# Kernel optimization log

Hardware: AMD Instinct MI355X
Metric: run time of the kernel (lower is better)

Reference implementation:

```python
import jax, jax.numpy as jnp
import numpy as np

H, C = 4, 32  # heads, per-head out_channels; hidden = H*C = 128


def _gatv2(x, Wl, bl, Wr, br, att, b, src, dst):
    """One PyG GATv2Conv layer (concat=True, add_self_loops=False, slope=0.2)."""
    N = x.shape[0]
    xl = (x @ Wl + bl).reshape(N, H, C)  # source transform (messages)
    xr = (x @ Wr + br).reshape(N, H, C)  # target transform
    msg = xl[src]                         # [E,H,C] gather per edge
    e = jax.nn.leaky_relu(msg + xr[dst], 0.2)
    a = jnp.einsum('ehc,hc->eh', e, att)  # [E,H] attention logits
    # segment softmax over incoming edges of each target node
    amax = jax.ops.segment_max(a, dst, num_segments=N)
    a = jnp.exp(a - amax[dst])
    denom = jax.ops.segment_sum(a, dst, num_segments=N)
    a = a / (denom[dst] + 1e-16)
    out = jax.ops.segment_sum(a[..., None] * msg, dst, num_segments=N)  # [N,H,C]
    return out.reshape(N, H * C) + b


def setup_inputs() -> dict:
    key = jax.random.key(0)
    ks = jax.random.split(key, 16)
    N, E, F = 50000, 800000, H * C
    s = 1.0 / np.sqrt(F)
    inp = {
        'x': jax.random.normal(ks[0], (N, F), dtype=jnp.float32),
        'edge_index': jax.random.randint(ks[1], (2, E), 0, N, dtype=jnp.int32),
    }
    names = ['Wl1', 'Wr1', 'Wl2', 'Wr2']
    for i, n in enumerate(names):
        inp[n] = jax.random.normal(ks[2 + i], (F, F), dtype=jnp.float32) * s
    inp['bl1'] = jnp.zeros((F,), jnp.float32)
    inp['br1'] = jnp.zeros((F,), jnp.float32)
    inp['bl2'] = jnp.zeros((F,), jnp.float32)
    inp['br2'] = jnp.zeros((F,), jnp.float32)
    inp['att1'] = jax.random.normal(ks[6], (H, C), dtype=jnp.float32) * s
    inp['att2'] = jax.random.normal(ks[7], (H, C), dtype=jnp.float32) * s
    inp['b1'] = jnp.zeros((F,), jnp.float32)
    inp['b2'] = jnp.zeros((F,), jnp.float32)
    return inp


def reference(x, edge_index, Wl1, bl1, Wr1, br1, att1, b1,
              Wl2, bl2, Wr2, br2, att2, b2):
    src, dst = edge_index[0], edge_index[1]
    h = jax.nn.relu(_gatv2(x, Wl1, bl1, Wr1, br1, att1, b1, src, dst))
    out = _gatv2(h, Wl2, bl2, Wr2, br2, att2, b2, src, dst)
    return out
```

## Files before the change

### kernel.cpp

```cpp
#include <hip/hip_runtime.h>
#include <hip/hip_bf16.h>
#include <hip/hip_fp16.h>
#include <float.h>

#define F 128
#define HEADS 4
#define CPH 32

#define NB 512
#define BSHIFT 7
#define G 64

using f16x2 = __attribute__((ext_vector_type(2))) _Float16;
using f16x8 = __attribute__((ext_vector_type(8))) _Float16;
using f32x4 = __attribute__((ext_vector_type(4))) float;


__global__ __launch_bounds__(1024) void hist_convw_kernel(
    const int* __restrict__ dst, int* __restrict__ counts, int E, int chunk,
    const float* __restrict__ W0, const float* __restrict__ W1,
    const float* __restrict__ W2, const float* __restrict__ W3,
    _Float16* __restrict__ T0, _Float16* __restrict__ T1,
    _Float16* __restrict__ T2, _Float16* __restrict__ T3)
{
    __shared__ int hist[NB];
    if (blockIdx.x < G) {
        int blk = blockIdx.x;
        for (int b = threadIdx.x; b < NB; b += 1024) hist[b] = 0;
        __syncthreads();
        int e0 = blk * chunk, e1 = min(e0 + chunk, E);
        for (int e = e0 + threadIdx.x; e < e1; e += 1024)
            atomicAdd(&hist[dst[e] >> BSHIFT], 1);
        __syncthreads();
        for (int b = threadIdx.x; b < NB; b += 1024)
            counts[b * G + blk] = hist[b];
    } else {
        int b = blockIdx.x - G;
        int m = b >> 4;
        int tid = (b & 15) * 1024 + threadIdx.x;
        int n = tid >> 7, k = tid & 127;
        const float* W = m == 0 ? W0 : m == 1 ? W1 : m == 2 ? W2 : W3;
        _Float16*    T = m == 0 ? T0 : m == 1 ? T1 : m == 2 ? T2 : T3;
        T[tid] = (_Float16)W[k * F + n];
    }
}


__global__ __launch_bounds__(1024) void scan_fused_kernel(
    const int* __restrict__ counts, int* __restrict__ offsets)
{
    __shared__ int tmp[1024];
    int t = threadIdx.x;
    int loc[32];
    int s = 0;
    #pragma unroll
    for (int j = 0; j < 32; ++j) { loc[j] = s; s += counts[t * 32 + j]; }
    tmp[t] = s;
    __syncthreads();
    for (int o = 1; o < 1024; o <<= 1) {
        int a = (t >= o) ? tmp[t - o] : 0;
        __syncthreads();
        tmp[t] += a;
        __syncthreads();
    }
    int excl = tmp[t] - s;
    #pragma unroll
    for (int j = 0; j < 32; ++j) offsets[t * 32 + j] = excl + loc[j];
}

__global__ __launch_bounds__(1024) void bucket_scatter_kernel(
    const int* __restrict__ src, const int* __restrict__ dst,
    const int* __restrict__ offsets, uint2* __restrict__ pairs, int E, int chunk)
{
    __shared__ int curs[NB];
    int blk = blockIdx.x;
    for (int b = threadIdx.x; b < NB; b += 1024) curs[b] = offsets[b * G + blk];
    __syncthreads();
    int e0 = blk * chunk, e1 = min(e0 + chunk, E);
    for (int e = e0 + threadIdx.x; e < e1; e += 1024) {
        int d = dst[e];
        int pos = atomicAdd(&curs[d >> BSHIFT], 1);
        pairs[pos] = make_uint2((unsigned)src[e], (unsigned)d);
    }
}

__global__ __launch_bounds__(256) void bucket_csr_kernel(
    const uint2* __restrict__ pairs, const int* __restrict__ offsets,
    int* __restrict__ row_ptr, int* __restrict__ srcs, int N, int E)
{
    int b = blockIdx.x;
    int seg0 = offsets[b * G];
    int seg1 = (b < NB - 1) ? offsets[(b + 1) * G] : E;
    __shared__ int hist[128], curs[128];
    if (threadIdx.x < 128) hist[threadIdx.x] = 0;
    __syncthreads();
    for (int e = seg0 + threadIdx.x; e < seg1; e += 256)
        atomicAdd(&hist[pairs[e].y & 127], 1);
    __syncthreads();
    int v = (threadIdx.x < 128) ? hist[threadIdx.x] : 0;
    if (threadIdx.x < 128) curs[threadIdx.x] = v;
    __syncthreads();
    for (int o = 1; o < 128; o <<= 1) {
        int a = 0;
        if (threadIdx.x < 128 && threadIdx.x >= o) a = curs[threadIdx.x - o];
        __syncthreads();
        if (threadIdx.x < 128) curs[threadIdx.x] += a;
        __syncthreads();
    }
    int excl = (threadIdx.x < 128) ? curs[threadIdx.x] - v : 0;
    __syncthreads();
    if (threadIdx.x < 128) {
        int node = b * 128 + threadIdx.x;
        if (node <= N) row_ptr[node] = seg0 + excl;
        curs[threadIdx.x] = excl;
    }
    __syncthreads();
    for (int e = seg0 + threadIdx.x; e < seg1; e += 256) {
        uint2 p = pairs[e];
        int pos = seg0 + atomicAdd(&curs[p.y & 127], 1);
        srcs[pos] = (int)p.x;
    }
}


template<int A_FP32>
__global__ __launch_bounds__(256) void mfma_gemm_kernel(
    const void* __restrict__ Xin,
    const _Float16* __restrict__ Wlt, const float* __restrict__ bl,
    const _Float16* __restrict__ Wrt, const float* __restrict__ br,
    _Float16* __restrict__ xl, float* __restrict__ xr, int N)
{
    const int m = blockIdx.y;
    const _Float16* Wt = m ? Wrt : Wlt;

    __shared__ f16x8 Ws[F * 17];
    for (int i = threadIdx.x; i < F * 16; i += 256) {
        int row = i >> 4, g = i & 15;
        Ws[row * 17 + g] = ((const f16x8*)Wt)[i];
    }
    __syncthreads();

    const int wid  = threadIdx.x >> 6;
    const int lane = threadIdx.x & 63;
    const int row0 = blockIdx.x * 64 + wid * 16;
    const int arow = lane & 15;
    const int g    = lane >> 4;

    int xrow = row0 + arow;
    if (xrow >= N) xrow = N - 1;
    f16x8 af[4];
    if (A_FP32) {
        const float* xp = (const float*)Xin + (size_t)xrow * F + g * 8;
        #pragma unroll
        for (int t = 0; t < 4; ++t) {
            float4 lo = *(const float4*)(xp + t * 32);
            float4 hi = *(const float4*)(xp + t * 32 + 4);
            f16x8 a;
            a[0] = (_Float16)lo.x; a[1] = (_Float16)lo.y; a[2] = (_Float16)lo.z; a[3] = (_Float16)lo.w;
            a[4] = (_Float16)hi.x; a[5] = (_Float16)hi.y; a[6] = (_Float16)hi.z; a[7] = (_Float16)hi.w;
            af[t] = a;
        }
    } else {
        const _Float16* xp = (const _Float16*)Xin + (size_t)xrow * F + g * 8;
        #pragma unroll
        for (int t = 0; t < 4; ++t)
            af[t] = *(const f16x8*)(xp + t * 32);
    }

    f32x4 acc[8];
    #pragma unroll
    for (int nt = 0; nt < 8; ++nt) acc[nt] = (f32x4){0.f, 0.f, 0.f, 0.f};

    #pragma unroll
    for (int t = 0; t < 4; ++t)
        #pragma unroll
        for (int nt = 0; nt < 8; ++nt) {
            f16x8 b = Ws[(nt * 16 + arow) * 17 + (t * 4 + g)];
            acc[nt] = __builtin_amdgcn_mfma_f32_16x16x32_f16(af[t], b, acc[nt], 0, 0, 0);
        }

    const float* bias = m ? br : bl;
    #pragma unroll
    for (int nt = 0; nt < 8; ++nt) {
        int ccol = nt * 16 + (lane & 15);
        float bv = bias[ccol];
        #pragma unroll
        for (int r2 = 0; r2 < 4; ++r2) {
            int crow = row0 + (lane >> 4) * 4 + r2;
            if (crow < N) {
                float v = acc[nt][r2] + bv;
                if (m == 0) xl[(size_t)crow * F + ccol] = (_Float16)v;
                else        xr[(size_t)crow * F + ccol] = v;
            }
        }
    }
}


__global__ __launch_bounds__(256) void gat_edge_kernel(
    const _Float16* __restrict__ xlh, const float* __restrict__ xr,
    const int* __restrict__ srcs, const int* __restrict__ row_ptr,
    const float* __restrict__ att, const float* __restrict__ bias,
    float* __restrict__ outf, _Float16* __restrict__ outh,
    int N, int do_relu, int out_half)
{
    int node = blockIdx.x * 4 + threadIdx.y;
    if (node >= N) return;
    int lane = threadIdx.x;
    int es = lane >> 4;
    int q  = lane & 15;

    const float* xrp = xr + (size_t)node * F + q * 8;
    float4 xa = *(const float4*)(xrp);
    float4 xb = *(const float4*)(xrp + 4);
    f16x2 xrh[4] = { {(_Float16)xa.x, (_Float16)xa.y}, {(_Float16)xa.z, (_Float16)xa.w},
                     {(_Float16)xb.x, (_Float16)xb.y}, {(_Float16)xb.z, (_Float16)xb.w} };
    float4 aa = *(const float4*)(att + q * 8);
    float4 ab = *(const float4*)(att + q * 8 + 4);
    f16x2 ath[4] = { {(_Float16)aa.x, (_Float16)aa.y}, {(_Float16)aa.z, (_Float16)aa.w},
                     {(_Float16)ab.x, (_Float16)ab.y}, {(_Float16)ab.z, (_Float16)ab.w} };
    const f16x2 slope = {(_Float16)0.2f, (_Float16)0.2f};

    int beg = row_ptr[node], end = row_ptr[node + 1];
    float s = 0.f;
    float o[8] = {0.f, 0.f, 0.f, 0.f, 0.f, 0.f, 0.f, 0.f};

    #pragma unroll 2
    for (int i = beg; i < end; i += 8) {
        int iA = i + es;       bool vA = iA < end;
        int iB = i + 4 + es;   bool vB = iB < end;
        int snA = srcs[vA ? iA : beg];
        int snB = srcs[vB ? iB : beg];
        f16x8 hA = *(const f16x8*)(xlh + (size_t)snA * F + q * 8);
        f16x8 hB = *(const f16x8*)(xlh + (size_t)snB * F + q * 8);
        const f16x2* a2 = (const f16x2*)&hA;
        const f16x2* b2 = (const f16x2*)&hB;

        f16x2 pA2 = {(_Float16)0.f, (_Float16)0.f};
        f16x2 pB2 = {(_Float16)0.f, (_Float16)0.f};
        #pragma unroll
        for (int j = 0; j < 4; ++j) {
            f16x2 eA = a2[j] + xrh[j];
            eA = __builtin_elementwise_max(eA, eA * slope);
            pA2 += eA * ath[j];
            f16x2 eB = b2[j] + xrh[j];
            eB = __builtin_elementwise_max(eB, eB * slope);
            pB2 += eB * ath[j];
        }
        float pA = (float)pA2[0] + (float)pA2[1];
        float pB = (float)pB2[0] + (float)pB2[1];
        pA += __shfl_xor(pA, 1); pA += __shfl_xor(pA, 2);
        pB += __shfl_xor(pB, 1); pB += __shfl_xor(pB, 2);
        float wA = vA ? __expf(pA) : 0.f;
        float wB = vB ? __expf(pB) : 0.f;
        s += wA + wB;
        #pragma unroll
        for (int j = 0; j < 8; ++j) {
            o[j] = fmaf(wA, (float)hA[j], o[j]);
            o[j] = fmaf(wB, (float)hB[j], o[j]);
        }
    }

    s += __shfl_xor(s, 16); s += __shfl_xor(s, 32);
    #pragma unroll
    for (int j = 0; j < 8; ++j) {
        o[j] += __shfl_xor(o[j], 16);
        o[j] += __shfl_xor(o[j], 32);
    }

    if (es == 0) {
        float inv = 1.f / (s + 1e-16f);
        float r[8];
        #pragma unroll
        for (int j = 0; j < 8; ++j) {
            r[j] = fmaf(o[j], inv, bias[q * 8 + j]);
            if (do_relu) r[j] = fmaxf(r[j], 0.f);
        }
        if (out_half) {
            f16x8 hv;
            #pragma unroll
            for (int j = 0; j < 8; ++j) hv[j] = (_Float16)r[j];
            *(f16x8*)(outh + (size_t)node * F + q * 8) = hv;
        } else {
            float4 lo = {r[0], r[1], r[2], r[3]};
            float4 hi = {r[4], r[5], r[6], r[7]};
            *(float4*)(outf + (size_t)node * F + q * 8) = lo;
            *(float4*)(outf + (size_t)node * F + q * 8 + 4) = hi;
        }
    }
}


extern "C" void kernel_launch(void* const* d_in, const int* in_sizes, int n_in,
                              void* d_out, int out_size, void* d_ws, size_t ws_size,
                              hipStream_t stream)
{
    const float* x    = (const float*)d_in[0];
    const int*   ei   = (const int*)d_in[1];
    const float* Wl1  = (const float*)d_in[2];
    const float* Wr1  = (const float*)d_in[3];
    const float* Wl2  = (const float*)d_in[4];
    const float* Wr2  = (const float*)d_in[5];
    const float* bl1  = (const float*)d_in[6];
    const float* br1  = (const float*)d_in[7];
    const float* bl2  = (const float*)d_in[8];
    const float* br2  = (const float*)d_in[9];
    const float* att1 = (const float*)d_in[10];
    const float* att2 = (const float*)d_in[11];
    const float* b1   = (const float*)d_in[12];
    const float* b2   = (const float*)d_in[13];

    const int N = in_sizes[0] / F;
    const int E = in_sizes[1] / 2;
    const int* src = ei;
    const int* dst = ei + E;

    char* ws = (char*)d_ws;
    size_t off = 0;
    auto alloc = [&](size_t bytes) -> void* {
        void* p = ws + off;
        off = (off + bytes + 255) & ~(size_t)255;
        return p;
    };
    _Float16* hh   = (_Float16*)alloc((size_t)N * F * sizeof(_Float16));
    _Float16* xlh  = (_Float16*)alloc((size_t)N * F * sizeof(_Float16));
    float*    xr   = (float*)alloc((size_t)N * F * sizeof(float));
    _Float16* Wt1l = (_Float16*)alloc((size_t)F * F * sizeof(_Float16));
    _Float16* Wt1r = (_Float16*)alloc((size_t)F * F * sizeof(_Float16));
    _Float16* Wt2l = (_Float16*)alloc((size_t)F * F * sizeof(_Float16));
    _Float16* Wt2r = (_Float16*)alloc((size_t)F * F * sizeof(_Float16));
    int*   row_ptr = (int*)alloc((size_t)(N + 1) * sizeof(int));
    int*   counts  = (int*)alloc((size_t)NB * G * sizeof(int));
    int*   offsets = (int*)alloc((size_t)NB * G * sizeof(int));
    uint2* pairs   = (uint2*)alloc((size_t)E * sizeof(uint2));
    int*   srcs    = (int*)alloc((size_t)E * sizeof(int));

    const int chunk = (E + G - 1) / G;
    hist_convw_kernel<<<G + 64, 1024, 0, stream>>>(dst, counts, E, chunk,
                                                   Wl1, Wr1, Wl2, Wr2,
                                                   Wt1l, Wt1r, Wt2l, Wt2r);
    scan_fused_kernel<<<1, 1024, 0, stream>>>(counts, offsets);
    bucket_scatter_kernel<<<G, 1024, 0, stream>>>(src, dst, offsets, pairs, E, chunk);
    bucket_csr_kernel<<<NB, 256, 0, stream>>>(pairs, offsets, row_ptr, srcs, N, E);

    const int gemm_blocks = (N + 63) / 64;
    dim3 gemm_grid(gemm_blocks, 2);
    dim3 eb(64, 4);
    const int edge_blocks = (N + 3) / 4;

    mfma_gemm_kernel<1><<<gemm_grid, 256, 0, stream>>>(
        x, Wt1l, bl1, Wt1r, br1, xlh, xr, N);
    gat_edge_kernel<<<edge_blocks, eb, 0, stream>>>(
        xlh, xr, srcs, row_ptr, att1, b1, nullptr, hh, N, 1, 1);

    mfma_gemm_kernel<0><<<gemm_grid, 256, 0, stream>>>(
        hh, Wt2l, bl2, Wt2r, br2, xlh, xr, N);
    gat_edge_kernel<<<edge_blocks, eb, 0, stream>>>(
        xlh, xr, srcs, row_ptr, att2, b2, (float*)d_out, nullptr, N, 0, 0);
}
```

Measured before the change: 167.6 us.

## Map one node per 16-lane group, store xr and att in fp16, pre-shift src offsets

The edge kernel now gives each node one 16-lane group instead of a full wavefront that split edges across four groups. This removes the cross-group shuffle reduction and the masked lanes. In exchange each group walks its edge list serially, two edges per step, and the edge kernel launches fewer waves. The target transform xr is now written and read as fp16, attention vectors are converted to fp16 once in the setup kernel, and the CSR source indices are stored pre-multiplied into byte offsets to save address arithmetic. The main risks are less memory-level parallelism per wave, more load imbalance from uneven node degrees, and slightly lower precision in xr.

```diff
diff --git a/kernel.cpp b/kernel.cpp
--- a/kernel.cpp
+++ b/kernel.cpp
@@ -21,7 +21,9 @@
     const float* __restrict__ W0, const float* __restrict__ W1,
     const float* __restrict__ W2, const float* __restrict__ W3,
     _Float16* __restrict__ T0, _Float16* __restrict__ T1,
-    _Float16* __restrict__ T2, _Float16* __restrict__ T3)
+    _Float16* __restrict__ T2, _Float16* __restrict__ T3,
+    const float* __restrict__ att1, const float* __restrict__ att2,
+    _Float16* __restrict__ attH1, _Float16* __restrict__ attH2)
 {
     __shared__ int hist[NB];
     if (blockIdx.x < G) {
@@ -34,7 +36,7 @@
         __syncthreads();
         for (int b = threadIdx.x; b < NB; b += 1024)
             counts[b * G + blk] = hist[b];
-    } else {
+    } else if (blockIdx.x < G + 64) {
         int b = blockIdx.x - G;
         int m = b >> 4;
         int tid = (b & 15) * 1024 + threadIdx.x;
@@ -42,6 +44,9 @@
         const float* W = m == 0 ? W0 : m == 1 ? W1 : m == 2 ? W2 : W3;
         _Float16*    T = m == 0 ? T0 : m == 1 ? T1 : m == 2 ? T2 : T3;
         T[tid] = (_Float16)W[k * F + n];
+    } else {
+        if (threadIdx.x < 128)      attH1[threadIdx.x] = (_Float16)att1[threadIdx.x];
+        else if (threadIdx.x < 256) attH2[threadIdx.x - 128] = (_Float16)att2[threadIdx.x - 128];
     }
 }
 
@@ -86,7 +91,7 @@
 
 __global__ __launch_bounds__(256) void bucket_csr_kernel(
     const uint2* __restrict__ pairs, const int* __restrict__ offsets,
-    int* __restrict__ row_ptr, int* __restrict__ srcs, int N, int E)
+    int* __restrict__ row_ptr, int* __restrict__ srcs8, int N, int E)
 {
     int b = blockIdx.x;
     int seg0 = offsets[b * G];
@@ -118,7 +123,7 @@
     for (int e = seg0 + threadIdx.x; e < seg1; e += 256) {
         uint2 p = pairs[e];
         int pos = seg0 + atomicAdd(&curs[p.y & 127], 1);
-        srcs[pos] = (int)p.x;
+        srcs8[pos] = (int)(p.x << 8);
     }
 }
 
@@ -128,7 +133,7 @@
     const void* __restrict__ Xin,
     const _Float16* __restrict__ Wlt, const float* __restrict__ bl,
     const _Float16* __restrict__ Wrt, const float* __restrict__ br,
-    _Float16* __restrict__ xl, float* __restrict__ xr, int N)
+    _Float16* __restrict__ xl, _Float16* __restrict__ xr, int N)
 {
     const int m = blockIdx.y;
     const _Float16* Wt = m ? Wrt : Wlt;
@@ -180,6 +185,7 @@
         }
 
     const float* bias = m ? br : bl;
+    _Float16* out = m ? xr : xl;
     #pragma unroll
     for (int nt = 0; nt < 8; ++nt) {
         int ccol = nt * 16 + (lane & 15);
@@ -187,52 +193,42 @@
         #pragma unroll
         for (int r2 = 0; r2 < 4; ++r2) {
             int crow = row0 + (lane >> 4) * 4 + r2;
-            if (crow < N) {
-                float v = acc[nt][r2] + bv;
-                if (m == 0) xl[(size_t)crow * F + ccol] = (_Float16)v;
-                else        xr[(size_t)crow * F + ccol] = v;
-            }
+            if (crow < N)
+                out[(size_t)crow * F + ccol] = (_Float16)(acc[nt][r2] + bv);
         }
     }
 }
 
 
 __global__ __launch_bounds__(256) void gat_edge_kernel(
-    const _Float16* __restrict__ xlh, const float* __restrict__ xr,
-    const int* __restrict__ srcs, const int* __restrict__ row_ptr,
-    const float* __restrict__ att, const float* __restrict__ bias,
+    const char* __restrict__ xlh_bytes, const _Float16* __restrict__ xrh,
+    const int* __restrict__ srcs8, const int* __restrict__ row_ptr,
+    const _Float16* __restrict__ attH, const float* __restrict__ bias,
     float* __restrict__ outf, _Float16* __restrict__ outh,
     int N, int do_relu, int out_half)
 {
-    int node = blockIdx.x * 4 + threadIdx.y;
+    int lane = threadIdx.x;
+    int grp  = lane >> 4;
+    int q    = lane & 15;
+    int node = blockIdx.x * 16 + threadIdx.y * 4 + grp;
     if (node >= N) return;
-    int lane = threadIdx.x;
-    int es = lane >> 4;
-    int q  = lane & 15;
-
-    const float* xrp = xr + (size_t)node * F + q * 8;
-    float4 xa = *(const float4*)(xrp);
-    float4 xb = *(const float4*)(xrp + 4);
-    f16x2 xrh[4] = { {(_Float16)xa.x, (_Float16)xa.y}, {(_Float16)xa.z, (_Float16)xa.w},
-                     {(_Float16)xb.x, (_Float16)xb.y}, {(_Float16)xb.z, (_Float16)xb.w} };
-    float4 aa = *(const float4*)(att + q * 8);
-    float4 ab = *(const float4*)(att + q * 8 + 4);
-    f16x2 ath[4] = { {(_Float16)aa.x, (_Float16)aa.y}, {(_Float16)aa.z, (_Float16)aa.w},
-                     {(_Float16)ab.x, (_Float16)ab.y}, {(_Float16)ab.z, (_Float16)ab.w} };
+
+    f16x8 xr8 = *(const f16x8*)(xrh + (size_t)node * F + q * 8);
+    f16x8 at8 = *(const f16x8*)(attH + q * 8);
+    const f16x2* xr2 = (const f16x2*)&xr8;
+    const f16x2* at2 = (const f16x2*)&at8;
     const f16x2 slope = {(_Float16)0.2f, (_Float16)0.2f};
 
     int beg = row_ptr[node], end = row_ptr[node + 1];
     float s = 0.f;
     float o[8] = {0.f, 0.f, 0.f, 0.f, 0.f, 0.f, 0.f, 0.f};
 
-    #pragma unroll 2
-    for (int i = beg; i < end; i += 8) {
-        int iA = i + es;       bool vA = iA < end;
-        int iB = i + 4 + es;   bool vB = iB < end;
-        int snA = srcs[vA ? iA : beg];
-        int snB = srcs[vB ? iB : beg];
-        f16x8 hA = *(const f16x8*)(xlh + (size_t)snA * F + q * 8);
-        f16x8 hB = *(const f16x8*)(xlh + (size_t)snB * F + q * 8);
+    for (int i = beg; i < end; i += 2) {
+        int offA = srcs8[i];
+        bool vB = (i + 1) < end;
+        int offB = srcs8[vB ? i + 1 : i];
+        f16x8 hA = *(const f16x8*)(xlh_bytes + (size_t)(unsigned)offA + q * 16);
+        f16x8 hB = *(const f16x8*)(xlh_bytes + (size_t)(unsigned)offB + q * 16);
         const f16x2* a2 = (const f16x2*)&hA;
         const f16x2* b2 = (const f16x2*)&hB;
 
@@ -240,18 +236,18 @@
         f16x2 pB2 = {(_Float16)0.f, (_Float16)0.f};
         #pragma unroll
         for (int j = 0; j < 4; ++j) {
-            f16x2 eA = a2[j] + xrh[j];
+            f16x2 eA = a2[j] + xr2[j];
             eA = __builtin_elementwise_max(eA, eA * slope);
-            pA2 += eA * ath[j];
-            f16x2 eB = b2[j] + xrh[j];
+            pA2 += eA * at2[j];
+            f16x2 eB = b2[j] + xr2[j];
             eB = __builtin_elementwise_max(eB, eB * slope);
-            pB2 += eB * ath[j];
+            pB2 += eB * at2[j];
         }
         float pA = (float)pA2[0] + (float)pA2[1];
         float pB = (float)pB2[0] + (float)pB2[1];
         pA += __shfl_xor(pA, 1); pA += __shfl_xor(pA, 2);
         pB += __shfl_xor(pB, 1); pB += __shfl_xor(pB, 2);
-        float wA = vA ? __expf(pA) : 0.f;
+        float wA = __expf(pA);
         float wB = vB ? __expf(pB) : 0.f;
         s += wA + wB;
         #pragma unroll
@@ -261,32 +257,23 @@
         }
     }
 
-    s += __shfl_xor(s, 16); s += __shfl_xor(s, 32);
+    float inv = 1.f / (s + 1e-16f);
+    float r[8];
     #pragma unroll
     for (int j = 0; j < 8; ++j) {
-        o[j] += __shfl_xor(o[j], 16);
-        o[j] += __shfl_xor(o[j], 32);
-    }
-
-    if (es == 0) {
-        float inv = 1.f / (s + 1e-16f);
-        float r[8];
-        #pragma unroll
-        for (int j = 0; j < 8; ++j) {
-            r[j] = fmaf(o[j], inv, bias[q * 8 + j]);
-            if (do_relu) r[j] = fmaxf(r[j], 0.f);
-        }
-        if (out_half) {
-            f16x8 hv;
-            #pragma unroll
-            for (int j = 0; j < 8; ++j) hv[j] = (_Float16)r[j];
-            *(f16x8*)(outh + (size_t)node * F + q * 8) = hv;
-        } else {
-            float4 lo = {r[0], r[1], r[2], r[3]};
-            float4 hi = {r[4], r[5], r[6], r[7]};
-            *(float4*)(outf + (size_t)node * F + q * 8) = lo;
-            *(float4*)(outf + (size_t)node * F + q * 8 + 4) = hi;
-        }
+        r[j] = fmaf(o[j], inv, bias[q * 8 + j]);
+        if (do_relu) r[j] = fmaxf(r[j], 0.f);
+    }
+    if (out_half) {
+        f16x8 hv;
+        #pragma unroll
+        for (int j = 0; j < 8; ++j) hv[j] = (_Float16)r[j];
+        *(f16x8*)(outh + (size_t)node * F + q * 8) = hv;
+    } else {
+        float4 lo = {r[0], r[1], r[2], r[3]};
+        float4 hi = {r[4], r[5], r[6], r[7]};
+        *(float4*)(outf + (size_t)node * F + q * 8) = lo;
+        *(float4*)(outf + (size_t)node * F + q * 8 + 4) = hi;
     }
 }
 
@@ -324,37 +311,42 @@
     };
     _Float16* hh   = (_Float16*)alloc((size_t)N * F * sizeof(_Float16));
     _Float16* xlh  = (_Float16*)alloc((size_t)N * F * sizeof(_Float16));
-    float*    xr   = (float*)alloc((size_t)N * F * sizeof(float));
+    _Float16* xrh  = (_Float16*)alloc((size_t)N * F * sizeof(_Float16));
     _Float16* Wt1l = (_Float16*)alloc((size_t)F * F * sizeof(_Float16));
     _Float16* Wt1r = (_Float16*)alloc((size_t)F * F * sizeof(_Float16));
     _Float16* Wt2l = (_Float16*)alloc((size_t)F * F * sizeof(_Float16));
     _Float16* Wt2r = (_Float16*)alloc((size_t)F * F * sizeof(_Float16));
+    _Float16* attH1 = (_Float16*)alloc(F * sizeof(_Float16));
+    _Float16* attH2 = (_Float16*)alloc(F * sizeof(_Float16));
     int*   row_ptr = (int*)alloc((size_t)(N + 1) * sizeof(int));
     int*   counts  = (int*)alloc((size_t)NB * G * sizeof(int));
     int*   offsets = (int*)alloc((size_t)NB * G * sizeof(int));
     uint2* pairs   = (uint2*)alloc((size_t)E * sizeof(uint2));
-    int*   srcs    = (int*)alloc((size_t)E * sizeof(int));
+    int*   srcs8   = (int*)alloc((size_t)E * sizeof(int));
 
     const int chunk = (E + G - 1) / G;
-    hist_convw_kernel<<<G + 64, 1024, 0, stream>>>(dst, counts, E, chunk,
+    hist_convw_kernel<<<G + 65, 1024, 0, stream>>>(dst, counts, E, chunk,
                                                    Wl1, Wr1, Wl2, Wr2,
-                                                   Wt1l, Wt1r, Wt2l, Wt2r);
+                                                   Wt1l, Wt1r, Wt2l, Wt2r,
+                                                   att1, att2, attH1, attH2);
     scan_fused_kernel<<<1, 1024, 0, stream>>>(counts, offsets);
     bucket_scatter_kernel<<<G, 1024, 0, stream>>>(src, dst, offsets, pairs, E, chunk);
-    bucket_csr_kernel<<<NB, 256, 0, stream>>>(pairs, offsets, row_ptr, srcs, N, E);
+    bucket_csr_kernel<<<NB, 256, 0, stream>>>(pairs, offsets, row_ptr, srcs8, N, E);
 
     const int gemm_blocks = (N + 63) / 64;
     dim3 gemm_grid(gemm_blocks, 2);
     dim3 eb(64, 4);
-    const int edge_blocks = (N + 3) / 4;
+    const int edge_blocks = (N + 15) / 16;
 
     mfma_gemm_kernel<1><<<gemm_grid, 256, 0, stream>>>(
-        x, Wt1l, bl1, Wt1r, br1, xlh, xr, N);
+        x, Wt1l, bl1, Wt1r, br1, xlh, xrh, N);
     gat_edge_kernel<<<edge_blocks, eb, 0, stream>>>(
-        xlh, xr, srcs, row_ptr, att1, b1, nullptr, hh, N, 1, 1);
+        (const char*)xlh, xrh, srcs8, row_ptr, attH1, b1,
+        nullptr, hh, N, 1, 1);
 
     mfma_gemm_kernel<0><<<gemm_grid, 256, 0, stream>>>(
-        hh, Wt2l, bl2, Wt2r, br2, xlh, xr, N);
+        hh, Wt2l, bl2, Wt2r, br2, xlh, xrh, N);
     gat_edge_kernel<<<edge_blocks, eb, 0, stream>>>(
-        xlh, xr, srcs, row_ptr, att2, b2, (float*)d_out, nullptr, N, 0, 0);
-}
+        (const char*)xlh, xrh, srcs8, row_ptr, attH2, b2,
+        (float*)d_out, nullptr, N, 0, 0);
+}
```

After: 157.9 us. -5.7%, faster.
